# Optimization experiments

Measured on AMD Instinct MI355X. Metric: run time of the kernel, lower is better.

Reference implementation:

```python
import jax, jax.numpy as jnp
import numpy as np

TEMPERATURE = 8.0  # sqrt(d_k) with d_k = 64
MASK_FILL = -65504.0  # fp16 min, as in the original


def setup_inputs() -> dict:
    key = jax.random.key(0)
    kq, kk, kv, km = jax.random.split(key, 4)
    BH, L, D = 16, 2048, 64
    q = jax.random.normal(kq, (BH, L, D), dtype=jnp.float32)
    k = jax.random.normal(kk, (BH, L, D), dtype=jnp.float32)
    v = jax.random.normal(kv, (BH, L, D), dtype=jnp.float32)
    mask = jax.random.randint(km, (BH, L, L), 0, 2).astype(jnp.bool_)
    return {"q": q, "k": k, "v": v, "mask": mask}


def reference(q, k, v, mask):
    # attn = q @ k^T / temperature, masked_fill, softmax over last dim
    attn = jnp.einsum("bqd,bkd->bqk", q, k) / TEMPERATURE
    attn = jnp.where(mask, MASK_FILL, attn)
    attn = jax.nn.softmax(attn, axis=2)
    # dropout with p=0.0 is identity (eval-mode reference)
    output = jnp.einsum("bqk,bkd->bqd", attn, v)
    return (output, attn)
```

## Files before the change

kernel.cpp:

```cpp
#include <hip/hip_runtime.h>

#define BH 16
#define L 2048
#define D 64
#define QB 64
#define KB 64
#define STRIDE 72
#define SCALE 0.125f
#define MASK_FILL -65504.0f

typedef __bf16 bf16x8 __attribute__((ext_vector_type(8)));
typedef float f32x4 __attribute__((ext_vector_type(4)));

__device__ __forceinline__ unsigned short f2bf(float f) {
    union { float f; unsigned u; } x; x.f = f;
    unsigned r = (x.u + 0x7FFFu + ((x.u >> 16) & 1u)) >> 16;
    return (unsigned short)r;
}
__device__ __forceinline__ float bf2f(unsigned short h) {
    union { unsigned u; float f; } x; x.u = ((unsigned)h) << 16;
    return x.f;
}

extern "C" __global__ __launch_bounds__(256, 2)
void sdpa_kernel(const float* __restrict__ q, const float* __restrict__ k,
                 const float* __restrict__ v, const int* __restrict__ mask,
                 float* __restrict__ out, float* __restrict__ attn)
{
    __shared__ unsigned short sQ[QB * STRIDE];
    __shared__ unsigned short sK[KB * STRIDE];
    __shared__ unsigned short sVt[D * STRIDE];
    __shared__ unsigned short sP[QB * STRIDE];
    __shared__ unsigned long long sM[QB * 33];

    const int tid  = threadIdx.x;
    const int lane = tid & 63;
    const int w    = tid >> 6;
    const int quad = lane >> 4;
    const int l15  = lane & 15;

    const int p  = blockIdx.x;
    const int bh = p & (BH - 1);
    const int qb = p >> 4;
    const int q0 = qb * QB;

    const size_t base = (size_t)bh * L * D;
    const float* Qb = q + base + (size_t)q0 * D;
    const float* Kb = k + base;
    const float* Vb = v + base;
    const int*   Mb = mask + (size_t)bh * L * L + (size_t)q0 * L;
    float*       Ab = attn + (size_t)bh * L * L + (size_t)q0 * L;
    float*       Ob = out  + base + (size_t)q0 * D;

    {
        const float2* Qs = (const float2*)Qb;
        for (int i = 0; i < 8; ++i) {
            int idx = i * 256 + tid;
            int row = idx >> 5;
            int d2  = idx & 31;
            float2 val = Qs[idx];
            unsigned pk = (unsigned)f2bf(val.x) | ((unsigned)f2bf(val.y) << 16);
            *(unsigned*)&sQ[row * STRIDE + d2 * 2] = pk;
        }
    }

    for (int rr = 0; rr < 16; ++rr) {
        int row = w * 16 + rr;
        const int4* Ms = (const int4*)(Mb + (size_t)row * L);
        for (int it = 0; it < 8; ++it) {
            int4 mv = Ms[it * 64 + lane];
            unsigned long long b0 = __ballot(mv.x != 0);
            unsigned long long b1 = __ballot(mv.y != 0);
            unsigned long long b2 = __ballot(mv.z != 0);
            unsigned long long b3 = __ballot(mv.w != 0);
            if (lane == 0) {
                unsigned long long* dst = &sM[row * 33 + it * 4];
                dst[0] = b0; dst[1] = b1; dst[2] = b2; dst[3] = b3;
            }
        }
    }
    __syncthreads();

    const int qrow = w * 16 + l15;
    bf16x8 qa0 = *(const bf16x8*)&sQ[qrow * STRIDE + quad * 8];
    bf16x8 qa1 = *(const bf16x8*)&sQ[qrow * STRIDE + quad * 8 + 32];

    float lsum[4] = {0.f, 0.f, 0.f, 0.f};
    for (int kt = 0; kt < L / KB; ++kt) {
        const int k0 = kt * KB;
        __syncthreads();
        {
            const float2* Ks = (const float2*)(Kb + (size_t)k0 * D);
            for (int i = 0; i < 8; ++i) {
                int idx = i * 256 + tid;
                int row = idx >> 5;
                int d2  = idx & 31;
                float2 val = Ks[idx];
                unsigned pk = (unsigned)f2bf(val.x) | ((unsigned)f2bf(val.y) << 16);
                *(unsigned*)&sK[row * STRIDE + d2 * 2] = pk;
            }
        }
        __syncthreads();

        f32x4 acc[4];
        for (int nt = 0; nt < 4; ++nt) {
            bf16x8 b0 = *(const bf16x8*)&sK[(nt * 16 + l15) * STRIDE + quad * 8];
            bf16x8 b1 = *(const bf16x8*)&sK[(nt * 16 + l15) * STRIDE + quad * 8 + 32];
            f32x4 c = {0.f, 0.f, 0.f, 0.f};
            c = __builtin_amdgcn_mfma_f32_16x16x32_bf16(qa0, b0, c, 0, 0, 0);
            c = __builtin_amdgcn_mfma_f32_16x16x32_bf16(qa1, b1, c, 0, 0, 0);
            acc[nt] = c;
        }
        const int widx  = (k0 >> 8) * 4 + (lane & 3);
        const int bsh0  = (k0 >> 2) + (l15 >> 2);
        for (int r = 0; r < 4; ++r) {
            int row = w * 16 + quad * 4 + r;
            unsigned long long mw = sM[row * 33 + widx];
            float s = 0.f;
            for (int nt = 0; nt < 4; ++nt) {
                float val = acc[nt][r] * SCALE;
                int bit = (int)((mw >> ((bsh0 + nt * 4) & 63)) & 1ull);
                val = bit ? MASK_FILL : val;
                s += __expf(val);
            }
            lsum[r] += s;
        }
    }
    for (int off = 1; off < 16; off <<= 1)
        for (int r = 0; r < 4; ++r)
            lsum[r] += __shfl_xor(lsum[r], off, 64);
    float rinv[4];
    for (int r = 0; r < 4; ++r) rinv[r] = 1.0f / lsum[r];

    f32x4 oacc[4];
    for (int nt = 0; nt < 4; ++nt) oacc[nt] = (f32x4){0.f, 0.f, 0.f, 0.f};

    for (int kt = 0; kt < L / KB; ++kt) {
        const int k0 = kt * KB;
        __syncthreads();
        {
            const float2* Ks = (const float2*)(Kb + (size_t)k0 * D);
            for (int i = 0; i < 8; ++i) {
                int idx = i * 256 + tid;
                int row = idx >> 5;
                int d2  = idx & 31;
                float2 val = Ks[idx];
                unsigned pk = (unsigned)f2bf(val.x) | ((unsigned)f2bf(val.y) << 16);
                *(unsigned*)&sK[row * STRIDE + d2 * 2] = pk;
            }
        }
        {
            unsigned pk[8];
            for (int jj = 0; jj < 16; ++jj) {
                float val = Vb[(size_t)(k0 + w * 16 + jj) * D + lane];
                unsigned short b = f2bf(val);
                if (jj & 1) pk[jj >> 1] |= ((unsigned)b) << 16;
                else        pk[jj >> 1]  = b;
            }
            uint4* dst = (uint4*)&sVt[lane * STRIDE + w * 16];
            dst[0] = make_uint4(pk[0], pk[1], pk[2], pk[3]);
            dst[1] = make_uint4(pk[4], pk[5], pk[6], pk[7]);
        }
        __syncthreads();

        f32x4 acc[4];
        for (int nt = 0; nt < 4; ++nt) {
            bf16x8 b0 = *(const bf16x8*)&sK[(nt * 16 + l15) * STRIDE + quad * 8];
            bf16x8 b1 = *(const bf16x8*)&sK[(nt * 16 + l15) * STRIDE + quad * 8 + 32];
            f32x4 c = {0.f, 0.f, 0.f, 0.f};
            c = __builtin_amdgcn_mfma_f32_16x16x32_bf16(qa0, b0, c, 0, 0, 0);
            c = __builtin_amdgcn_mfma_f32_16x16x32_bf16(qa1, b1, c, 0, 0, 0);
            acc[nt] = c;
        }
        const int widx = (k0 >> 8) * 4 + (lane & 3);
        const int bsh0 = (k0 >> 2) + (l15 >> 2);
        for (int r = 0; r < 4; ++r) {
            int row = w * 16 + quad * 4 + r;
            unsigned long long mw = sM[row * 33 + widx];
            for (int nt = 0; nt < 4; ++nt) {
                float val = acc[nt][r] * SCALE;
                int bit = (int)((mw >> ((bsh0 + nt * 4) & 63)) & 1ull);
                val = bit ? MASK_FILL : val;
                float pr = __expf(val) * rinv[r];
                sP[row * STRIDE + nt * 16 + l15] = f2bf(pr);
            }
        }
        for (int it = 0; it < 4; ++it) {
            int row = w * 16 + it * 4 + quad;
            unsigned long long pv = *(const unsigned long long*)&sP[row * STRIDE + l15 * 4];
            float4 o;
            o.x = bf2f((unsigned short)(pv         & 0xFFFF));
            o.y = bf2f((unsigned short)((pv >> 16) & 0xFFFF));
            o.z = bf2f((unsigned short)((pv >> 32) & 0xFFFF));
            o.w = bf2f((unsigned short)((pv >> 48) & 0xFFFF));
            *(float4*)&Ab[(size_t)row * L + k0 + l15 * 4] = o;
        }
        {
            bf16x8 pa0 = *(const bf16x8*)&sP[qrow * STRIDE + quad * 8];
            bf16x8 pa1 = *(const bf16x8*)&sP[qrow * STRIDE + quad * 8 + 32];
            for (int nt = 0; nt < 4; ++nt) {
                bf16x8 vb0 = *(const bf16x8*)&sVt[(nt * 16 + l15) * STRIDE + quad * 8];
                bf16x8 vb1 = *(const bf16x8*)&sVt[(nt * 16 + l15) * STRIDE + quad * 8 + 32];
                oacc[nt] = __builtin_amdgcn_mfma_f32_16x16x32_bf16(pa0, vb0, oacc[nt], 0, 0, 0);
                oacc[nt] = __builtin_amdgcn_mfma_f32_16x16x32_bf16(pa1, vb1, oacc[nt], 0, 0, 0);
            }
        }
    }

    for (int nt = 0; nt < 4; ++nt)
        for (int r = 0; r < 4; ++r)
            Ob[(size_t)(w * 16 + quad * 4 + r) * D + nt * 16 + l15] = oacc[nt][r];
}

extern "C" void kernel_launch(void* const* d_in, const int* in_sizes, int n_in,
                              void* d_out, int out_size, void* d_ws, size_t ws_size,
                              hipStream_t stream)
{
    const float* q    = (const float*)d_in[0];
    const float* k    = (const float*)d_in[1];
    const float* v    = (const float*)d_in[2];
    const int*   mask = (const int*)d_in[3];
    float* out  = (float*)d_out;
    float* attn = out + (size_t)BH * L * D;

    dim3 grid(BH * (L / QB));
    dim3 block(256);
    hipLaunchKernelGGL(sdpa_kernel, grid, block, 0, stream,
                       q, k, v, mask, out, attn);
}
```

Measured before the change: 615.1 us.

## Precompute bf16 K/Vt and packed mask bits in workspace, async-load into LDS

```diff
diff --git a/kernel.cpp b/kernel.cpp
--- a/kernel.cpp
+++ b/kernel.cpp
@@ -3,35 +3,258 @@
 #define BH 16
 #define L 2048
 #define D 64
-#define QB 64
+#define QB 32
 #define KB 64
-#define STRIDE 72
+#define NKT (L / KB)
 #define SCALE 0.125f
 #define MASK_FILL -65504.0f
 
 typedef __bf16 bf16x8 __attribute__((ext_vector_type(8)));
 typedef float f32x4 __attribute__((ext_vector_type(4)));
 
-__device__ __forceinline__ unsigned short f2bf(float f) {
+__device__ __forceinline__ unsigned f2bf(float f) {
     union { float f; unsigned u; } x; x.f = f;
-    unsigned r = (x.u + 0x7FFFu + ((x.u >> 16) & 1u)) >> 16;
-    return (unsigned short)r;
+    return (x.u + 0x7FFFu + ((x.u >> 16) & 1u)) >> 16;
 }
 __device__ __forceinline__ float bf2f(unsigned short h) {
     union { unsigned u; float f; } x; x.u = ((unsigned)h) << 16;
     return x.f;
 }
+
+__device__ __forceinline__ void gload16(const void* g, void* l) {
+    __builtin_amdgcn_global_load_lds(
+        (const __attribute__((address_space(1))) unsigned int*)g,
+        (__attribute__((address_space(3))) unsigned int*)l, 16, 0, 0);
+}
+
+
+extern "C" __global__ __launch_bounds__(256)
+void preK(const float* __restrict__ k, uint4* __restrict__ wsK)
+{
+    int idx = blockIdx.x * 256 + threadIdx.x;
+    int c   = idx & 7;
+    int key = (idx >> 3) & (L - 1);
+    int bh  = idx >> 14;
+    const float4* src = (const float4*)(k + ((size_t)(bh * L + key) * D + c * 8));
+    float4 a = src[0], b = src[1];
+    uint4 o;
+    o.x = f2bf(a.x) | (f2bf(a.y) << 16);
+    o.y = f2bf(a.z) | (f2bf(a.w) << 16);
+    o.z = f2bf(b.x) | (f2bf(b.y) << 16);
+    o.w = f2bf(b.z) | (f2bf(b.w) << 16);
+    wsK[(size_t)(bh * L + key) * 8 + (c ^ (key & 7))] = o;
+}
+
+extern "C" __global__ __launch_bounds__(256)
+void preV(const float* __restrict__ v, uint4* __restrict__ wsVt)
+{
+    __shared__ float sT[64 * 68];
+    int b = blockIdx.x;
+    int bh = b >> 5, kt = b & 31;
+    const float4* src = (const float4*)(v + ((size_t)bh * L + kt * 64) * D);
+    int t = threadIdx.x;
+    #pragma unroll
+    for (int i = 0; i < 4; ++i) {
+        int i4 = i * 256 + t;
+        int key = i4 >> 4, c4 = i4 & 15;
+        float4 val = src[i4];
+        *(float4*)&sT[key * 68 + c4 * 4] = val;
+    }
+    __syncthreads();
+    int d = t >> 2, cg = t & 3;
+    #pragma unroll
+    for (int j = 0; j < 2; ++j) {
+        int c = cg + j * 4;
+        unsigned pk[4];
+        #pragma unroll
+        for (int e = 0; e < 4; ++e) {
+            float x0 = sT[(c * 8 + e * 2    ) * 68 + d];
+            float x1 = sT[(c * 8 + e * 2 + 1) * 68 + d];
+            pk[e] = f2bf(x0) | (f2bf(x1) << 16);
+        }
+        wsVt[((size_t)(bh * 32 + kt) * 64 + d) * 8 + (c ^ (d & 7))] =
+            make_uint4(pk[0], pk[1], pk[2], pk[3]);
+    }
+}
+
+extern "C" __global__ __launch_bounds__(256)
+void preM(const int* __restrict__ mask, unsigned long long* __restrict__ wsM)
+{
+    __shared__ unsigned long long sW[16 * 32];
+    int b = blockIdx.x;
+    size_t row0 = (size_t)b * 16;
+    int w = threadIdx.x >> 6, lane = threadIdx.x & 63;
+    const int* src = mask + row0 * L;
+    for (int rr = 0; rr < 4; ++rr) {
+        int r = w * 4 + rr;
+        #pragma unroll 8
+        for (int wd = 0; wd < 32; ++wd) {
+            int val = src[(size_t)r * L + wd * 64 + lane];
+            unsigned long long bal = __ballot(val != 0);
+            if (lane == 0) sW[r * 32 + wd] = bal;
+        }
+    }
+    __syncthreads();
+    int t = threadIdx.x;
+    ((uint4*)wsM)[(size_t)b * 256 + t] = ((const uint4*)sW)[t];
+}
+
+
+extern "C" __global__ __launch_bounds__(256, 4)
+void sdpa_main(const float* __restrict__ q, const uint4* __restrict__ gKall,
+               const uint4* __restrict__ gVall, const unsigned long long* __restrict__ wsM,
+               float* __restrict__ out, float* __restrict__ attn)
+{
+    __shared__ unsigned short sK[2][KB * 64];
+    __shared__ unsigned short sVt[2][D * 64];
+    __shared__ unsigned short sP[QB * 72];
+    __shared__ float sPart[4][16];
+
+    const int tid = threadIdx.x, lane = tid & 63, w = tid >> 6;
+    const int wr = w & 1, wn = w >> 1;
+    const int quad = lane >> 4, l15 = lane & 15;
+    const int p = blockIdx.x, bh = p & 15, qb = p >> 4, q0 = qb * QB;
+
+    const uint4* gK = gKall + (size_t)bh * L * 8;
+    const uint4* gV = gVall + (size_t)bh * L * 8;
+
+    const float* Qp = q + (size_t)(bh * L + q0 + wr * 16 + l15) * D + quad * 8;
+    float4 qv0 = *(const float4*)(Qp);
+    float4 qv1 = *(const float4*)(Qp + 4);
+    float4 qv2 = *(const float4*)(Qp + 32);
+    float4 qv3 = *(const float4*)(Qp + 36);
+    union { bf16x8 v; unsigned short s[8]; } qa0u, qa1u;
+    qa0u.s[0] = f2bf(qv0.x); qa0u.s[1] = f2bf(qv0.y); qa0u.s[2] = f2bf(qv0.z); qa0u.s[3] = f2bf(qv0.w);
+    qa0u.s[4] = f2bf(qv1.x); qa0u.s[5] = f2bf(qv1.y); qa0u.s[6] = f2bf(qv1.z); qa0u.s[7] = f2bf(qv1.w);
+    qa1u.s[0] = f2bf(qv2.x); qa1u.s[1] = f2bf(qv2.y); qa1u.s[2] = f2bf(qv2.z); qa1u.s[3] = f2bf(qv2.w);
+    qa1u.s[4] = f2bf(qv3.x); qa1u.s[5] = f2bf(qv3.y); qa1u.s[6] = f2bf(qv3.z); qa1u.s[7] = f2bf(qv3.w);
+    const bf16x8 qa0 = qa0u.v, qa1 = qa1u.v;
+
+    const unsigned long long* Mw = wsM + (size_t)(bh * L + q0 + wr * 16 + quad * 4) * 32;
+
+    auto stageK = [&](int kt, int buf) {
+        const uint4* s = gK + (size_t)kt * 512 + w * 128 + lane;
+        gload16(s,      &sK[buf][(w * 128) * 8]);
+        gload16(s + 64, &sK[buf][(w * 128 + 64) * 8]);
+    };
+    auto stageV = [&](int kt, int buf) {
+        const uint4* s = gV + (size_t)kt * 512 + w * 128 + lane;
+        gload16(s,      &sVt[buf][(w * 128) * 8]);
+        gload16(s + 64, &sVt[buf][(w * 128 + 64) * 8]);
+    };
+    auto scompute = [&](int cur, f32x4* acc) {
+        #pragma unroll
+        for (int j = 0; j < 2; ++j) {
+            int key = (wn * 2 + j) * 16 + l15;
+            const bf16x8 b0 = *(const bf16x8*)&sK[cur][key * 64 + ((quad     ^ (key & 7)) * 8)];
+            const bf16x8 b1 = *(const bf16x8*)&sK[cur][key * 64 + (((quad+4) ^ (key & 7)) * 8)];
+            f32x4 c = {0.f, 0.f, 0.f, 0.f};
+            c = __builtin_amdgcn_mfma_f32_16x16x32_bf16(qa0, b0, c, 0, 0, 0);
+            c = __builtin_amdgcn_mfma_f32_16x16x32_bf16(qa1, b1, c, 0, 0, 0);
+            acc[j] = c;
+        }
+    };
+
+    float lsum[4] = {0.f, 0.f, 0.f, 0.f};
+    stageK(0, 0);
+    __syncthreads();
+    for (int kt = 0; kt < NKT; ++kt) {
+        int cur = kt & 1;
+        if (kt + 1 < NKT) stageK(kt + 1, cur ^ 1);
+        unsigned long long mw[4];
+        #pragma unroll
+        for (int r = 0; r < 4; ++r) mw[r] = Mw[r * 32 + kt];
+        f32x4 acc[2];
+        scompute(cur, acc);
+        #pragma unroll
+        for (int j = 0; j < 2; ++j) {
+            int sh = (wn * 2 + j) * 16 + l15;
+            #pragma unroll
+            for (int r = 0; r < 4; ++r) {
+                float val = acc[j][r] * SCALE;
+                val = ((mw[r] >> sh) & 1ull) ? MASK_FILL : val;
+                lsum[r] += __expf(val);
+            }
+        }
+        __syncthreads();
+    }
+    #pragma unroll
+    for (int off = 1; off < 16; off <<= 1)
+        #pragma unroll
+        for (int r = 0; r < 4; ++r) lsum[r] += __shfl_xor(lsum[r], off, 64);
+    if (l15 == 0) {
+        #pragma unroll
+        for (int r = 0; r < 4; ++r) sPart[w][quad * 4 + r] = lsum[r];
+    }
+    __syncthreads();
+    float rinv[4];
+    #pragma unroll
+    for (int r = 0; r < 4; ++r)
+        rinv[r] = 1.0f / (sPart[wr][quad * 4 + r] + sPart[wr + 2][quad * 4 + r]);
+
+    f32x4 oacc[2];
+    oacc[0] = (f32x4){0.f, 0.f, 0.f, 0.f};
+    oacc[1] = (f32x4){0.f, 0.f, 0.f, 0.f};
+    float* Ab = attn + ((size_t)bh * L + q0) * L;
+
+    stageK(0, 0); stageV(0, 0);
+    __syncthreads();
+    for (int kt = 0; kt < NKT; ++kt) {
+        int cur = kt & 1;
+        if (kt + 1 < NKT) { stageK(kt + 1, cur ^ 1); stageV(kt + 1, cur ^ 1); }
+        unsigned long long mw[4];
+        #pragma unroll
+        for (int r = 0; r < 4; ++r) mw[r] = Mw[r * 32 + kt];
+        f32x4 acc[2];
+        scompute(cur, acc);
+        #pragma unroll
+        for (int j = 0; j < 2; ++j) {
+            int col = (wn * 2 + j) * 16 + l15;
+            #pragma unroll
+            for (int r = 0; r < 4; ++r) {
+                float val = acc[j][r] * SCALE;
+                val = ((mw[r] >> col) & 1ull) ? MASK_FILL : val;
+                float pr = __expf(val) * rinv[r];
+                int row = wr * 16 + quad * 4 + r;
+                Ab[(size_t)row * L + kt * 64 + col] = pr;
+                sP[row * 72 + col] = (unsigned short)f2bf(pr);
+            }
+        }
+        __syncthreads();
+        {
+            const bf16x8 pa0 = *(const bf16x8*)&sP[(wr * 16 + l15) * 72 + quad * 8];
+            const bf16x8 pa1 = *(const bf16x8*)&sP[(wr * 16 + l15) * 72 + quad * 8 + 32];
+            #pragma unroll
+            for (int j = 0; j < 2; ++j) {
+                int dd = (wn * 2 + j) * 16 + l15;
+                const bf16x8 vb0 = *(const bf16x8*)&sVt[cur][dd * 64 + ((quad     ^ (dd & 7)) * 8)];
+                const bf16x8 vb1 = *(const bf16x8*)&sVt[cur][dd * 64 + (((quad+4) ^ (dd & 7)) * 8)];
+                oacc[j] = __builtin_amdgcn_mfma_f32_16x16x32_bf16(pa0, vb0, oacc[j], 0, 0, 0);
+                oacc[j] = __builtin_amdgcn_mfma_f32_16x16x32_bf16(pa1, vb1, oacc[j], 0, 0, 0);
+            }
+        }
+        __syncthreads();
+    }
+
+    float* Ob = out + ((size_t)bh * L + q0) * D;
+    #pragma unroll
+    for (int j = 0; j < 2; ++j)
+        #pragma unroll
+        for (int r = 0; r < 4; ++r)
+            Ob[(size_t)(wr * 16 + quad * 4 + r) * D + (wn * 2 + j) * 16 + l15] = oacc[j][r];
+}
+
 
 extern "C" __global__ __launch_bounds__(256, 2)
 void sdpa_kernel(const float* __restrict__ q, const float* __restrict__ k,
                  const float* __restrict__ v, const int* __restrict__ mask,
                  float* __restrict__ out, float* __restrict__ attn)
 {
-    __shared__ unsigned short sQ[QB * STRIDE];
-    __shared__ unsigned short sK[KB * STRIDE];
-    __shared__ unsigned short sVt[D * STRIDE];
-    __shared__ unsigned short sP[QB * STRIDE];
-    __shared__ unsigned long long sM[QB * 33];
+    __shared__ unsigned short fQ[64 * 72];
+    __shared__ unsigned short fK[64 * 72];
+    __shared__ unsigned short fVt[64 * 72];
+    __shared__ unsigned short fP[64 * 72];
+    __shared__ unsigned long long fM[64 * 33];
 
     const int tid  = threadIdx.x;
     const int lane = tid & 63;
@@ -42,7 +265,7 @@
     const int p  = blockIdx.x;
     const int bh = p & (BH - 1);
     const int qb = p >> 4;
-    const int q0 = qb * QB;
+    const int q0 = qb * 64;
 
     const size_t base = (size_t)bh * L * D;
     const float* Qb = q + base + (size_t)q0 * D;
@@ -56,14 +279,12 @@
         const float2* Qs = (const float2*)Qb;
         for (int i = 0; i < 8; ++i) {
             int idx = i * 256 + tid;
-            int row = idx >> 5;
-            int d2  = idx & 31;
+            int row = idx >> 5, d2 = idx & 31;
             float2 val = Qs[idx];
-            unsigned pk = (unsigned)f2bf(val.x) | ((unsigned)f2bf(val.y) << 16);
-            *(unsigned*)&sQ[row * STRIDE + d2 * 2] = pk;
-        }
-    }
-
+            unsigned pk = f2bf(val.x) | (f2bf(val.y) << 16);
+            *(unsigned*)&fQ[row * 72 + d2 * 2] = pk;
+        }
+    }
     for (int rr = 0; rr < 16; ++rr) {
         int row = w * 16 + rr;
         const int4* Ms = (const int4*)(Mb + (size_t)row * L);
@@ -74,7 +295,7 @@
             unsigned long long b2 = __ballot(mv.z != 0);
             unsigned long long b3 = __ballot(mv.w != 0);
             if (lane == 0) {
-                unsigned long long* dst = &sM[row * 33 + it * 4];
+                unsigned long long* dst = &fM[row * 33 + it * 4];
                 dst[0] = b0; dst[1] = b1; dst[2] = b2; dst[3] = b3;
             }
         }
@@ -82,44 +303,42 @@
     __syncthreads();
 
     const int qrow = w * 16 + l15;
-    bf16x8 qa0 = *(const bf16x8*)&sQ[qrow * STRIDE + quad * 8];
-    bf16x8 qa1 = *(const bf16x8*)&sQ[qrow * STRIDE + quad * 8 + 32];
+    bf16x8 qa0 = *(const bf16x8*)&fQ[qrow * 72 + quad * 8];
+    bf16x8 qa1 = *(const bf16x8*)&fQ[qrow * 72 + quad * 8 + 32];
 
     float lsum[4] = {0.f, 0.f, 0.f, 0.f};
-    for (int kt = 0; kt < L / KB; ++kt) {
-        const int k0 = kt * KB;
+    for (int kt = 0; kt < 32; ++kt) {
+        const int k0 = kt * 64;
         __syncthreads();
         {
             const float2* Ks = (const float2*)(Kb + (size_t)k0 * D);
             for (int i = 0; i < 8; ++i) {
                 int idx = i * 256 + tid;
-                int row = idx >> 5;
-                int d2  = idx & 31;
+                int row = idx >> 5, d2 = idx & 31;
                 float2 val = Ks[idx];
-                unsigned pk = (unsigned)f2bf(val.x) | ((unsigned)f2bf(val.y) << 16);
-                *(unsigned*)&sK[row * STRIDE + d2 * 2] = pk;
-            }
-        }
-        __syncthreads();
-
+                unsigned pk = f2bf(val.x) | (f2bf(val.y) << 16);
+                *(unsigned*)&fK[row * 72 + d2 * 2] = pk;
+            }
+        }
+        __syncthreads();
         f32x4 acc[4];
         for (int nt = 0; nt < 4; ++nt) {
-            bf16x8 b0 = *(const bf16x8*)&sK[(nt * 16 + l15) * STRIDE + quad * 8];
-            bf16x8 b1 = *(const bf16x8*)&sK[(nt * 16 + l15) * STRIDE + quad * 8 + 32];
+            bf16x8 b0 = *(const bf16x8*)&fK[(nt * 16 + l15) * 72 + quad * 8];
+            bf16x8 b1 = *(const bf16x8*)&fK[(nt * 16 + l15) * 72 + quad * 8 + 32];
             f32x4 c = {0.f, 0.f, 0.f, 0.f};
             c = __builtin_amdgcn_mfma_f32_16x16x32_bf16(qa0, b0, c, 0, 0, 0);
             c = __builtin_amdgcn_mfma_f32_16x16x32_bf16(qa1, b1, c, 0, 0, 0);
             acc[nt] = c;
         }
-        const int widx  = (k0 >> 8) * 4 + (lane & 3);
-        const int bsh0  = (k0 >> 2) + (l15 >> 2);
+        const int widx = (k0 >> 8) * 4 + (lane & 3);
+        const int bsh0 = (k0 >> 2) + (l15 >> 2);
         for (int r = 0; r < 4; ++r) {
             int row = w * 16 + quad * 4 + r;
-            unsigned long long mw = sM[row * 33 + widx];
+            unsigned long long mwv = fM[row * 33 + widx];
             float s = 0.f;
             for (int nt = 0; nt < 4; ++nt) {
                 float val = acc[nt][r] * SCALE;
-                int bit = (int)((mw >> ((bsh0 + nt * 4) & 63)) & 1ull);
+                int bit = (int)((mwv >> ((bsh0 + nt * 4) & 63)) & 1ull);
                 val = bit ? MASK_FILL : val;
                 s += __expf(val);
             }
@@ -127,46 +346,43 @@
         }
     }
     for (int off = 1; off < 16; off <<= 1)
-        for (int r = 0; r < 4; ++r)
-            lsum[r] += __shfl_xor(lsum[r], off, 64);
+        for (int r = 0; r < 4; ++r) lsum[r] += __shfl_xor(lsum[r], off, 64);
     float rinv[4];
     for (int r = 0; r < 4; ++r) rinv[r] = 1.0f / lsum[r];
 
     f32x4 oacc[4];
     for (int nt = 0; nt < 4; ++nt) oacc[nt] = (f32x4){0.f, 0.f, 0.f, 0.f};
 
-    for (int kt = 0; kt < L / KB; ++kt) {
-        const int k0 = kt * KB;
+    for (int kt = 0; kt < 32; ++kt) {
+        const int k0 = kt * 64;
         __syncthreads();
         {
             const float2* Ks = (const float2*)(Kb + (size_t)k0 * D);
             for (int i = 0; i < 8; ++i) {
                 int idx = i * 256 + tid;
-                int row = idx >> 5;
-                int d2  = idx & 31;
+                int row = idx >> 5, d2 = idx & 31;
                 float2 val = Ks[idx];
-                unsigned pk = (unsigned)f2bf(val.x) | ((unsigned)f2bf(val.y) << 16);
-                *(unsigned*)&sK[row * STRIDE + d2 * 2] = pk;
+                unsigned pk = f2bf(val.x) | (f2bf(val.y) << 16);
+                *(unsigned*)&fK[row * 72 + d2 * 2] = pk;
             }
         }
         {
             unsigned pk[8];
             for (int jj = 0; jj < 16; ++jj) {
                 float val = Vb[(size_t)(k0 + w * 16 + jj) * D + lane];
-                unsigned short b = f2bf(val);
-                if (jj & 1) pk[jj >> 1] |= ((unsigned)b) << 16;
-                else        pk[jj >> 1]  = b;
-            }
-            uint4* dst = (uint4*)&sVt[lane * STRIDE + w * 16];
+                unsigned bv = f2bf(val);
+                if (jj & 1) pk[jj >> 1] |= bv << 16;
+                else        pk[jj >> 1]  = bv;
+            }
+            uint4* dst = (uint4*)&fVt[lane * 72 + w * 16];
             dst[0] = make_uint4(pk[0], pk[1], pk[2], pk[3]);
             dst[1] = make_uint4(pk[4], pk[5], pk[6], pk[7]);
         }
         __syncthreads();
-
         f32x4 acc[4];
         for (int nt = 0; nt < 4; ++nt) {
-            bf16x8 b0 = *(const bf16x8*)&sK[(nt * 16 + l15) * STRIDE + quad * 8];
-            bf16x8 b1 = *(const bf16x8*)&sK[(nt * 16 + l15) * STRIDE + quad * 8 + 32];
+            bf16x8 b0 = *(const bf16x8*)&fK[(nt * 16 + l15) * 72 + quad * 8];
+            bf16x8 b1 = *(const bf16x8*)&fK[(nt * 16 + l15) * 72 + quad * 8 + 32];
             f32x4 c = {0.f, 0.f, 0.f, 0.f};
             c = __builtin_amdgcn_mfma_f32_16x16x32_bf16(qa0, b0, c, 0, 0, 0);
             c = __builtin_amdgcn_mfma_f32_16x16x32_bf16(qa1, b1, c, 0, 0, 0);
@@ -176,18 +392,18 @@
         const int bsh0 = (k0 >> 2) + (l15 >> 2);
         for (int r = 0; r < 4; ++r) {
             int row = w * 16 + quad * 4 + r;
-            unsigned long long mw = sM[row * 33 + widx];
+            unsigned long long mwv = fM[row * 33 + widx];
             for (int nt = 0; nt < 4; ++nt) {
                 float val = acc[nt][r] * SCALE;
-                int bit = (int)((mw >> ((bsh0 + nt * 4) & 63)) & 1ull);
+                int bit = (int)((mwv >> ((bsh0 + nt * 4) & 63)) & 1ull);
                 val = bit ? MASK_FILL : val;
                 float pr = __expf(val) * rinv[r];
-                sP[row * STRIDE + nt * 16 + l15] = f2bf(pr);
+                fP[row * 72 + nt * 16 + l15] = (unsigned short)f2bf(pr);
             }
         }
         for (int it = 0; it < 4; ++it) {
             int row = w * 16 + it * 4 + quad;
-            unsigned long long pv = *(const unsigned long long*)&sP[row * STRIDE + l15 * 4];
+            unsigned long long pv = *(const unsigned long long*)&fP[row * 72 + l15 * 4];
             float4 o;
             o.x = bf2f((unsigned short)(pv         & 0xFFFF));
             o.y = bf2f((unsigned short)((pv >> 16) & 0xFFFF));
@@ -196,21 +412,21 @@
             *(float4*)&Ab[(size_t)row * L + k0 + l15 * 4] = o;
         }
         {
-            bf16x8 pa0 = *(const bf16x8*)&sP[qrow * STRIDE + quad * 8];
-            bf16x8 pa1 = *(const bf16x8*)&sP[qrow * STRIDE + quad * 8 + 32];
+            bf16x8 pa0 = *(const bf16x8*)&fP[qrow * 72 + quad * 8];
+            bf16x8 pa1 = *(const bf16x8*)&fP[qrow * 72 + quad * 8 + 32];
             for (int nt = 0; nt < 4; ++nt) {
-                bf16x8 vb0 = *(const bf16x8*)&sVt[(nt * 16 + l15) * STRIDE + quad * 8];
-                bf16x8 vb1 = *(const bf16x8*)&sVt[(nt * 16 + l15) * STRIDE + quad * 8 + 32];
+                bf16x8 vb0 = *(const bf16x8*)&fVt[(nt * 16 + l15) * 72 + quad * 8];
+                bf16x8 vb1 = *(const bf16x8*)&fVt[(nt * 16 + l15) * 72 + quad * 8 + 32];
                 oacc[nt] = __builtin_amdgcn_mfma_f32_16x16x32_bf16(pa0, vb0, oacc[nt], 0, 0, 0);
                 oacc[nt] = __builtin_amdgcn_mfma_f32_16x16x32_bf16(pa1, vb1, oacc[nt], 0, 0, 0);
             }
         }
     }
-
     for (int nt = 0; nt < 4; ++nt)
         for (int r = 0; r < 4; ++r)
             Ob[(size_t)(w * 16 + quad * 4 + r) * D + nt * 16 + l15] = oacc[nt][r];
 }
+
 
 extern "C" void kernel_launch(void* const* d_in, const int* in_sizes, int n_in,
                               void* d_out, int out_size, void* d_ws, size_t ws_size,
@@ -223,8 +439,22 @@
     float* out  = (float*)d_out;
     float* attn = out + (size_t)BH * L * D;
 
-    dim3 grid(BH * (L / QB));
-    dim3 block(256);
-    hipLaunchKernelGGL(sdpa_kernel, grid, block, 0, stream,
-                       q, k, v, mask, out, attn);
-}
+    const size_t WS_K  = 0;
+    const size_t WS_VT = (size_t)BH * L * D * 2;
+    const size_t WS_M  = WS_VT + (size_t)BH * L * D * 2;
+    const size_t NEED  = WS_M + (size_t)BH * L * 32 * 8;
+
+    if (ws_size >= NEED) {
+        uint4* wsK  = (uint4*)((char*)d_ws + WS_K);
+        uint4* wsVt = (uint4*)((char*)d_ws + WS_VT);
+        unsigned long long* wsM = (unsigned long long*)((char*)d_ws + WS_M);
+        hipLaunchKernelGGL(preK, dim3(1024), dim3(256), 0, stream, k, wsK);
+        hipLaunchKernelGGL(preV, dim3(512),  dim3(256), 0, stream, v, wsVt);
+        hipLaunchKernelGGL(preM, dim3(2048), dim3(256), 0, stream, mask, wsM);
+        hipLaunchKernelGGL(sdpa_main, dim3(BH * (L / QB)), dim3(256), 0, stream,
+                           q, (const uint4*)wsK, (const uint4*)wsVt, wsM, out, attn);
+    } else {
+        hipLaunchKernelGGL(sdpa_kernel, dim3(BH * (L / 64)), dim3(256), 0, stream,
+                           q, k, v, mask, out, attn);
+    }
+}
```

Result: faster. 601.9 us (-2.1%).
